# Kernel tuning notes

Hardware: AMD Instinct MI355X
Metric: run time of the kernel (lower is better)

## Reference

```python
import jax, jax.numpy as jnp
import numpy as np

B, S, D = 1, 2048, 2048
H = 16            # num query heads
QL = 1536         # q_lora_rank
KVL = 512         # kv_lora_rank
DN = 128          # qk_nope_head_dim
DR = 64           # qk_rope_head_dim
DV = 128          # v_head_dim
F = 8192          # ffn intermediate
EPS = 1e-6
WAVE = 10000.0


def _rms(x, scale, eps=EPS):
    # fp32 norm then cast back, matching DeepSeekV3_1RMSNorm
    x32 = x.astype(jnp.float32)
    ms = jnp.mean(x32 * x32, axis=-1, keepdims=True)
    return (x32 * jax.lax.rsqrt(ms + eps)).astype(x.dtype) * scale


def _rope_tables(seq_len, dim):
    inv_freq = 1.0 / (WAVE ** (jnp.arange(0, dim, 2, dtype=jnp.float32) / dim))
    t = jnp.arange(seq_len, dtype=jnp.float32)[:, None] * inv_freq[None, :]  # [S, dim/2]
    emb = jnp.concatenate([t, t], axis=-1)  # [S, dim]
    return jnp.cos(emb), jnp.sin(emb)


def _apply_rope(x, cos, sin):
    # x: [B, S, H, dr]; rotate-half convention
    half = x.shape[-1] // 2
    x1, x2 = x[..., :half], x[..., half:]
    rot = jnp.concatenate([-x2, x1], axis=-1)
    return x * cos[None, :, None, :] + rot * sin[None, :, None, :]


def setup_inputs() -> dict:
    key = jax.random.key(0)
    ks = jax.random.split(key, 12)
    w = lambda k, shp: (jax.random.normal(k, shp, dtype=jnp.float32) * 0.02)
    inp = {
        "hidden_states": jax.random.normal(ks[0], (B, S, D), dtype=jnp.float32),
        "attention_mask": jnp.broadcast_to(jnp.tril(jnp.ones((S, S), dtype=bool)), (B, S, S)),
        "pre_attn_scale": jnp.ones((D,), jnp.float32),
        "wqa": w(ks[1], (D, QL)),
        "q_norm_scale": jnp.ones((QL,), jnp.float32),
        "wqb": w(ks[2], (QL, H * (DN + DR))),
        "wkva": w(ks[3], (D, KVL + DR)),
        "kv_norm_scale": jnp.ones((KVL,), jnp.float32),
        "wkvb": w(ks[4], (KVL, H * (DN + DV))),
        "wo": w(ks[5], (H * DV, D)),
        "pre_ffn_scale": jnp.ones((D,), jnp.float32),
        "wg": w(ks[6], (D, F)),
        "bg": jnp.zeros((F,), jnp.float32),
        "wu": w(ks[7], (D, F)),
        "bu": jnp.zeros((F,), jnp.float32),
        "wd": w(ks[8], (F, D)),
        "bd": jnp.zeros((D,), jnp.float32),
    }
    return inp


def reference(hidden_states, attention_mask, pre_attn_scale, wqa, q_norm_scale, wqb,
              wkva, kv_norm_scale, wkvb, wo, pre_ffn_scale, wg, bg, wu, bu, wd, bd):
    x = hidden_states
    # --- pre-attention RMSNorm ---
    n = _rms(x, pre_attn_scale)
    # --- MLA attention ---
    q = (_rms(n @ wqa, q_norm_scale) @ wqb).reshape(B, S, H, DN + DR)
    q_nope, q_rope = q[..., :DN], q[..., DN:]
    kva = n @ wkva                              # [B,S,KVL+DR]
    c_kv, k_rope = kva[..., :KVL], kva[..., KVL:]
    kv = (_rms(c_kv, kv_norm_scale) @ wkvb).reshape(B, S, H, DN + DV)
    k_nope, v = kv[..., :DN], kv[..., DN:]
    cos, sin = _rope_tables(S, DR)
    q_rope = _apply_rope(q_rope, cos, sin)
    k_rope = _apply_rope(k_rope[:, :, None, :], cos, sin)  # [B,S,1,DR] shared across heads
    qf = jnp.concatenate([q_nope, q_rope], axis=-1)
    kf = jnp.concatenate([k_nope, jnp.broadcast_to(k_rope, (B, S, H, DR))], axis=-1)
    scale = 1.0 / float(np.sqrt(DN + DR))
    scores = jnp.einsum('bqhd,bkhd->bhqk', qf, kf) * scale
    scores = jnp.where(attention_mask[:, None, :, :], scores, jnp.float32(-1e9))
    probs = jax.nn.softmax(scores, axis=-1)
    attn = jnp.einsum('bhqk,bkhd->bqhd', probs, v).reshape(B, S, H * DV)
    x = x + attn @ wo                            # residual 1 (dropout=0)
    # --- pre-FFN RMSNorm + dense SwiGLU FFN ---
    n = _rms(x, pre_ffn_scale)
    ff = (jax.nn.silu(n @ wg + bg) * (n @ wu + bu)) @ wd + bd
    return x + ff                                # residual 2
```

## Files before the change

### kernel.cpp

```cpp
#include <hip/hip_runtime.h>
#include <hip/hip_bf16.h>
#include <stdint.h>

typedef unsigned short u16;
using f32x4  = __attribute__((ext_vector_type(4))) float;
using bf16x8 = __attribute__((ext_vector_type(8))) __bf16;
using u32x4  = __attribute__((ext_vector_type(4))) uint32_t;
using u16x4  = __attribute__((ext_vector_type(4))) unsigned short;
using u16x8  = __attribute__((ext_vector_type(8))) unsigned short;

#define S_LEN 2048
#define DM    2048
#define NH    16
#define QLR   1536
#define KVLR  512
#define DNOPE 128
#define DROPE 64
#define DVAL  128
#define FFD   8192

static __device__ __forceinline__ float bf2f(u16 u) {
    union { uint32_t i; float f; } v; v.i = ((uint32_t)u) << 16; return v.f;
}
static __device__ __forceinline__ u16 f2bf(float f) {
    union { float f; uint32_t i; } v; v.f = f;
    uint32_t x = v.i;
    return (u16)((x + 0x7FFF + ((x >> 16) & 1)) >> 16);
}
static __device__ __forceinline__ void gload16(const u16* g, const u16* l) {
    __builtin_amdgcn_global_load_lds(
        (const __attribute__((address_space(1))) void*)g,
        (__attribute__((address_space(3))) void*)l, 16, 0, 0);
}

struct TWJob { const float* src; u16* dst; int R, C, xt, start; };
struct TWJobs { TWJob j[8]; };

__global__ __launch_bounds__(256)
void transpose_all(TWJobs jobs)
{
    __shared__ __align__(16) u16 tile[64][68];
    const int bid = blockIdx.x;
    int e = 0;
#pragma unroll
    for (int i = 1; i < 8; ++i) e = (bid >= jobs.j[i].start) ? i : e;
    const float* src = jobs.j[e].src;
    u16* dst = jobs.j[e].dst;
    const int R = jobs.j[e].R, C = jobs.j[e].C;
    const int local = bid - jobs.j[e].start;
    const int c0 = (local % jobs.j[e].xt) * 64;
    const int r0 = (local / jobs.j[e].xt) * 64;
    const int t = threadIdx.x;
#pragma unroll
    for (int i = 0; i < 4; ++i) {
        int idx = i * 256 + t;
        int r = idx >> 4, c4 = idx & 15;
        float4 v = *reinterpret_cast<const float4*>(&src[(size_t)(r0 + r) * C + c0 + c4 * 4]);
        u16x4 b; b[0] = f2bf(v.x); b[1] = f2bf(v.y); b[2] = f2bf(v.z); b[3] = f2bf(v.w);
        *reinterpret_cast<u16x4*>(&tile[r][c4 * 4]) = b;
    }
    __syncthreads();
#pragma unroll
    for (int i = 0; i < 4; ++i) {
        int idx = i * 256 + t;
        int rr = idx >> 4, k4 = idx & 15;
        u16x4 o;
#pragma unroll
        for (int j = 0; j < 4; ++j) o[j] = tile[k4 * 4 + j][rr];
        *reinterpret_cast<u16x4*>(&dst[(size_t)(c0 + rr) * R + r0 + k4 * 4]) = o;
    }
}

__global__ __launch_bounds__(256)
void transpose_v(const u16* __restrict__ kv, u16* __restrict__ vt)
{
    __shared__ __align__(16) u16 tile[64][76];
    const int t = threadIdx.x;
    const int s0 = blockIdx.x * 64;
    const int d0 = blockIdx.y * 64;
    const int h  = blockIdx.z;
#pragma unroll
    for (int i = 0; i < 2; ++i) {
        int idx = i * 256 + t;
        int s = idx >> 3, c8 = idx & 7;
        u16x8 v = *reinterpret_cast<const u16x8*>(kv + (size_t)(s0 + s) * (NH * 256) + h * 256 + 128 + d0 + c8 * 8);
        u16x4 lo, hi;
#pragma unroll
        for (int j = 0; j < 4; ++j) { lo[j] = v[j]; hi[j] = v[4 + j]; }
        *reinterpret_cast<u16x4*>(&tile[s][c8 * 8])     = lo;
        *reinterpret_cast<u16x4*>(&tile[s][c8 * 8 + 4]) = hi;
    }
    __syncthreads();
#pragma unroll
    for (int i = 0; i < 4; ++i) {
        int idx = i * 256 + t;
        int d = idx >> 4, s4 = idx & 15;
        u16x4 o;
#pragma unroll
        for (int j = 0; j < 4; ++j) o[j] = tile[s4 * 4 + j][d];
        *reinterpret_cast<u16x4*>(&vt[(size_t)(h * 128 + d0 + d) * S_LEN + s0 + s4 * 4]) = o;
    }
}

template<bool IN_F32>
__global__ __launch_bounds__(256)
void rms_norm(const void* __restrict__ in, int in_stride, int width,
              const float* __restrict__ scale, u16* __restrict__ out, int out_stride)
{
    const int row = blockIdx.x;
    const int t = threadIdx.x;
    const float* inf = (const float*)in;
    const u16*   inb = (const u16*)in;
    float ss = 0.f;
    for (int c = t; c < width; c += 256) {
        float v = IN_F32 ? inf[(size_t)row * in_stride + c] : bf2f(inb[(size_t)row * in_stride + c]);
        ss += v * v;
    }
#pragma unroll
    for (int o = 32; o > 0; o >>= 1) ss += __shfl_xor(ss, o);
    __shared__ float red[4];
    if ((t & 63) == 0) red[t >> 6] = ss;
    __syncthreads();
    float inv = rsqrtf((red[0] + red[1] + red[2] + red[3]) / (float)width + 1e-6f);
    for (int c = t; c < width; c += 256) {
        float v = IN_F32 ? inf[(size_t)row * in_stride + c] : bf2f(inb[(size_t)row * in_stride + c]);
        out[(size_t)row * out_stride + c] = f2bf(v * inv * scale[c]);
    }
}

__global__ __launch_bounds__(256)
void rope_qk(u16* __restrict__ q, const float* __restrict__ kva, u16* __restrict__ kr)
{
    const int s = blockIdx.x;
    const int t = threadIdx.x;
    for (int idx = t; idx < 544; idx += 256) {
        int d = idx & 31;
        float invf = powf(10000.f, -(float)(2 * d) / 64.f);
        float ang = (float)s * invf;
        float cs = cosf(ang), sn = sinf(ang);
        if (idx < 512) {
            int hh = idx >> 5;
            u16* base = q + ((size_t)s * NH + hh) * 192 + 128;
            float x1 = bf2f(base[d]), x2 = bf2f(base[d + 32]);
            base[d]      = f2bf(x1 * cs - x2 * sn);
            base[d + 32] = f2bf(x2 * cs + x1 * sn);
        } else {
            const float* kb = kva + (size_t)s * 576 + 512;
            float x1 = kb[d], x2 = kb[d + 32];
            kr[(size_t)s * 64 + d]      = f2bf(x1 * cs - x2 * sn);
            kr[(size_t)s * 64 + d + 32] = f2bf(x2 * cs + x1 * sn);
        }
    }
}

__global__ __launch_bounds__(256)
void init_out(const float* __restrict__ x2, const float* __restrict__ bd,
              float* __restrict__ out, int total4, int N)
{
    int i = blockIdx.x * 256 + threadIdx.x;
    const int stride = gridDim.x * 256;
    for (; i < total4; i += stride) {
        float4 r = ((const float4*)x2)[i];
        int col = (i * 4) & (N - 1);
        float4 b = *reinterpret_cast<const float4*>(&bd[col]);
        float4 o; o.x = r.x + b.x; o.y = r.y + b.y; o.z = r.z + b.z; o.w = r.w + b.w;
        ((float4*)out)[i] = o;
    }
}

__global__ __launch_bounds__(256)
void mul_gu(const u16* __restrict__ g, const u16* __restrict__ u,
            u16* __restrict__ h, int total8)
{
    int i = blockIdx.x * 256 + threadIdx.x;
    const int stride = gridDim.x * 256;
    for (; i < total8; i += stride) {
        u16x8 gv = ((const u16x8*)g)[i];
        u16x8 uv = ((const u16x8*)u)[i];
        u16x8 hv;
#pragma unroll
        for (int j = 0; j < 8; ++j) hv[j] = f2bf(bf2f(gv[j]) * bf2f(uv[j]));
        ((u16x8*)h)[i] = hv;
    }
}

struct GJob { const u16* A; const u16* BT; void* out; int N, K, yCount, zCount; };

template<int EPI>
__global__ __launch_bounds__(256)
void gemm_bt2(GJob j0, GJob j1)
{
    __shared__ __align__(16) u16 As[128 * 64];
    __shared__ __align__(16) u16 Bs[128 * 64];
    const int t = threadIdx.x;
    const int lane = t & 63;
    const int w = t >> 6;
    const int wr = w >> 1, wc = w & 1;
    const int li = lane & 15;
    const int lg = lane >> 4;

    const int gx = gridDim.x;
    int nwg = gx * gridDim.y;
    int bid = blockIdx.y * gx + blockIdx.x;
    bid = (bid & 7) * (nwg >> 3) + (bid >> 3);
    const int m0 = (bid % gx) * 128;
    int yy = bid / gx;

    const int j0span = j0.yCount * j0.zCount;
    const GJob& J = (yy < j0span) ? j0 : j1;
    if (yy >= j0span) yy -= j0span;
    const int ntile = yy % J.yCount;
    const int z = yy / J.yCount;
    const int n0 = ntile * 128;
    const int N = J.N, K = J.K;

    const int nktt = K >> 6;
    const int nz = J.zCount;
    const int qq = nktt / nz, rr = nktt % nz;
    const int kt0 = z * qq + (z < rr ? z : rr);
    const int ktEnd = kt0 + qq + (z < rr ? 1 : 0);

    const int srow = w * 32 + (lane >> 3);
    const int scol = (((lane & 7) ^ (lane >> 3)) << 3);
    const u16* ag = J.A  + (size_t)(m0 + srow) * K + scol;
    const u16* bg = J.BT + (size_t)(n0 + srow) * K + scol;

    f32x4 acc[4][4];
#pragma unroll
    for (int m = 0; m < 4; ++m)
#pragma unroll
        for (int n = 0; n < 4; ++n)
            acc[m][n] = f32x4{0.f, 0.f, 0.f, 0.f};

    for (int kt = kt0; kt < ktEnd; ++kt) {
        const int k0 = kt << 6;
        __syncthreads();
#pragma unroll
        for (int i = 0; i < 4; ++i) {
            gload16(ag + (size_t)i * 8 * K + k0, As + (w * 32 + i * 8) * 64);
            gload16(bg + (size_t)i * 8 * K + k0, Bs + (w * 32 + i * 8) * 64);
        }
        __syncthreads();
#pragma unroll
        for (int kk = 0; kk < 2; ++kk) {
            const int csw = (kk * 32 + lg * 8) ^ ((li & 7) << 3);
            bf16x8 af[4], bfr[4];
#pragma unroll
            for (int m = 0; m < 4; ++m)
                af[m] = *reinterpret_cast<const bf16x8*>(As + (wr * 64 + m * 16 + li) * 64 + csw);
#pragma unroll
            for (int n = 0; n < 4; ++n)
                bfr[n] = *reinterpret_cast<const bf16x8*>(Bs + (wc * 64 + n * 16 + li) * 64 + csw);
#pragma unroll
            for (int m = 0; m < 4; ++m)
#pragma unroll
                for (int n = 0; n < 4; ++n)
                    acc[m][n] = __builtin_amdgcn_mfma_f32_16x16x32_bf16(af[m], bfr[n], acc[m][n], 0, 0, 0);
        }
    }

#pragma unroll
    for (int m = 0; m < 4; ++m) {
        const int row = m0 + wr * 64 + m * 16 + lg * 4;
#pragma unroll
        for (int n = 0; n < 4; ++n) {
            const int col = n0 + wc * 64 + n * 16 + li;
            if (col < N) {
#pragma unroll
                for (int r2 = 0; r2 < 4; ++r2) {
                    float v = acc[m][n][r2];
                    size_t idx = (size_t)(row + r2) * N + col;
                    if (EPI == 0) ((u16*)J.out)[idx] = f2bf(v);
                    else          unsafeAtomicAdd((float*)J.out + idx, v);
                }
            }
        }
    }
}

template<int EPI>
__global__ __launch_bounds__(512, 4)
void gemm_big(const u16* __restrict__ A, const u16* __restrict__ BT,
              void* __restrict__ out, int M, int N, int K,
              const float* __restrict__ bias, const u16* __restrict__ gmul)
{
    __shared__ __align__(16) u16 As[256 * 64];
    __shared__ __align__(16) u16 Bs[128 * 64];
    const int t = threadIdx.x;
    const int lane = t & 63;
    const int w = t >> 6;
    const int wr = w >> 1, wc = w & 1;
    const int li = lane & 15;
    const int lg = lane >> 4;

    const int gx = gridDim.x;
    int nwg = gx * gridDim.y;
    int bid = blockIdx.y * gx + blockIdx.x;
    bid = (bid & 7) * (nwg >> 3) + (bid >> 3);
    const int m0 = (bid % gx) * 256;
    const int n0 = (bid / gx) * 128;

    const int nz = gridDim.z, z = blockIdx.z;
    const int nktt = K >> 6;
    const int qq = nktt / nz, rr = nktt % nz;
    const int kt0 = z * qq + (z < rr ? z : rr);
    const int ktEnd = kt0 + qq + (z < rr ? 1 : 0);

    const int sr = lane >> 3;
    const int scol = (((lane & 7) ^ sr) << 3);
    const u16* ag = A  + (size_t)(m0 + w * 8 + sr) * K + scol;
    const u16* bg = BT + (size_t)(n0 + w * 8 + sr) * K + scol;
    const u16* lA = As + (w * 8) * 64;
    const u16* lB = Bs + (w * 8) * 64;

    f32x4 acc[4][4];
#pragma unroll
    for (int m = 0; m < 4; ++m)
#pragma unroll
        for (int n = 0; n < 4; ++n)
            acc[m][n] = f32x4{0.f, 0.f, 0.f, 0.f};

    for (int kt = kt0; kt < ktEnd; ++kt) {
        const int k0 = kt << 6;
        __syncthreads();
#pragma unroll
        for (int i = 0; i < 4; ++i)
            gload16(ag + (size_t)i * 64 * K + k0, lA + i * 64 * 64);
#pragma unroll
        for (int i = 0; i < 2; ++i)
            gload16(bg + (size_t)i * 64 * K + k0, lB + i * 64 * 64);
        __syncthreads();
        __builtin_amdgcn_s_setprio(1);
#pragma unroll
        for (int kk = 0; kk < 2; ++kk) {
            const int csw = (kk * 32 + lg * 8) ^ ((li & 7) << 3);
            bf16x8 af[4], bfr[4];
#pragma unroll
            for (int m = 0; m < 4; ++m)
                af[m] = *reinterpret_cast<const bf16x8*>(As + (wr * 64 + m * 16 + li) * 64 + csw);
#pragma unroll
            for (int n = 0; n < 4; ++n)
                bfr[n] = *reinterpret_cast<const bf16x8*>(Bs + (wc * 64 + n * 16 + li) * 64 + csw);
#pragma unroll
            for (int m = 0; m < 4; ++m)
#pragma unroll
                for (int n = 0; n < 4; ++n)
                    acc[m][n] = __builtin_amdgcn_mfma_f32_16x16x32_bf16(af[m], bfr[n], acc[m][n], 0, 0, 0);
        }
        __builtin_amdgcn_s_setprio(0);
    }

#pragma unroll
    for (int m = 0; m < 4; ++m) {
        const int row = m0 + wr * 64 + m * 16 + lg * 4;
#pragma unroll
        for (int n = 0; n < 4; ++n) {
            const int col = n0 + wc * 64 + n * 16 + li;
#pragma unroll
            for (int r2 = 0; r2 < 4; ++r2) {
                float v = acc[m][n][r2];
                size_t idx = (size_t)(row + r2) * N + col;
                if (EPI == 0) {
                    ((u16*)out)[idx] = f2bf(v);
                } else if (EPI == 1) {
                    v += bias[col];
                    v = v / (1.f + __expf(-v));
                    ((u16*)out)[idx] = f2bf(v);
                } else {
                    unsafeAtomicAdd((float*)out + idx, v);
                }
            }
        }
    }
}

__global__ __launch_bounds__(512, 4)
void gemm_gu(const u16* __restrict__ A, const u16* __restrict__ BgT, const u16* __restrict__ BuT,
             u16* __restrict__ gout, u16* __restrict__ uout, int M, int N, int K,
             const float* __restrict__ bg, const float* __restrict__ bu)
{
    __shared__ __align__(16) u16 As[256 * 64];
    __shared__ __align__(16) u16 Bs[128 * 64];
    const int t = threadIdx.x;
    const int lane = t & 63;
    const int w = t >> 6;
    const int wr = w >> 1, wc = w & 1;
    const int li = lane & 15;
    const int lg = lane >> 4;
    const int isUp = blockIdx.z;

    const u16* BT = isUp ? BuT : BgT;
    const float* bias = isUp ? bu : bg;
    u16* out = isUp ? uout : gout;

    const int gx = gridDim.x;
    int nwg = gx * gridDim.y;
    int bid = blockIdx.y * gx + blockIdx.x;
    bid = (bid & 7) * (nwg >> 3) + (bid >> 3);
    const int m0 = (bid % gx) * 256;
    const int n0 = (bid / gx) * 128;

    const int sr = lane >> 3;
    const int scol = (((lane & 7) ^ sr) << 3);
    const u16* ag = A  + (size_t)(m0 + w * 8 + sr) * K + scol;
    const u16* bgp = BT + (size_t)(n0 + w * 8 + sr) * K + scol;
    const u16* lA = As + (w * 8) * 64;
    const u16* lB = Bs + (w * 8) * 64;

    f32x4 acc[4][4];
#pragma unroll
    for (int m = 0; m < 4; ++m)
#pragma unroll
        for (int n = 0; n < 4; ++n)
            acc[m][n] = f32x4{0.f, 0.f, 0.f, 0.f};

    const int nkt = K >> 6;
    for (int kt = 0; kt < nkt; ++kt) {
        const int k0 = kt << 6;
        __syncthreads();
#pragma unroll
        for (int i = 0; i < 4; ++i)
            gload16(ag + (size_t)i * 64 * K + k0, lA + i * 64 * 64);
#pragma unroll
        for (int i = 0; i < 2; ++i)
            gload16(bgp + (size_t)i * 64 * K + k0, lB + i * 64 * 64);
        __syncthreads();
        __builtin_amdgcn_s_setprio(1);
#pragma unroll
        for (int kk = 0; kk < 2; ++kk) {
            const int csw = (kk * 32 + lg * 8) ^ ((li & 7) << 3);
            bf16x8 af[4], bfr[4];
#pragma unroll
            for (int m = 0; m < 4; ++m)
                af[m] = *reinterpret_cast<const bf16x8*>(As + (wr * 64 + m * 16 + li) * 64 + csw);
#pragma unroll
            for (int n = 0; n < 4; ++n)
                bfr[n] = *reinterpret_cast<const bf16x8*>(Bs + (wc * 64 + n * 16 + li) * 64 + csw);
#pragma unroll
            for (int m = 0; m < 4; ++m)
#pragma unroll
                for (int n = 0; n < 4; ++n)
                    acc[m][n] = __builtin_amdgcn_mfma_f32_16x16x32_bf16(af[m], bfr[n], acc[m][n], 0, 0, 0);
        }
        __builtin_amdgcn_s_setprio(0);
    }

#pragma unroll
    for (int m = 0; m < 4; ++m) {
        const int row = m0 + wr * 64 + m * 16 + lg * 4;
#pragma unroll
        for (int n = 0; n < 4; ++n) {
            const int col = n0 + wc * 64 + n * 16 + li;
            float bv = bias[col];
#pragma unroll
            for (int r2 = 0; r2 < 4; ++r2) {
                float v = acc[m][n][r2] + bv;
                if (!isUp) v = v / (1.f + __expf(-v));
                ((u16*)out)[(size_t)(row + r2) * N + col] = f2bf(v);
            }
        }
    }
}

__global__ __launch_bounds__(512)
void flash_attn(const u16* __restrict__ q, const u16* __restrict__ kv,
                const u16* __restrict__ kr, const u16* __restrict__ vt,
                u16* __restrict__ attn)
{
    __shared__ __align__(16) u16 KVs[2][20480];
    __shared__ __align__(16) u16 Ps[8][16][72];

    const int t = threadIdx.x;
    const int lane = t & 63;
    const int w = t >> 6;
    const int li = lane & 15;
    const int lg = lane >> 4;
    const int h = blockIdx.x;
    const int b = 15 - blockIdx.y;

    const int qt = (w < 4) ? (2 * b + 1) : (2 * b);
    const int my_nkt = qt + 1;
    const int block_nkt = 2 * b + 2;
    const int wl = w & 3;
    const int qr = qt * 64 + wl * 16;
    const int qpos = qr + li;

    auto stage = [&](int buf, int k0) {
        u16* base = &KVs[buf][0];
#pragma unroll
        for (int i = 0; i < 3; ++i) {
            int g = w * 3 + i;
            int P = g * 64 + lane;
            int j = P / 24, s = P % 24;
            int c = (s & 24) | ((s ^ (j & 7)) & 7);
            const u16* src = (c < 16)
                ? kv + (size_t)(k0 + j) * (NH * 256) + h * 256 + c * 8
                : kr + (size_t)(k0 + j) * 64 + (c - 16) * 8;
            gload16(src, base + g * 512);
        }
#pragma unroll
        for (int i = 0; i < 2; ++i) {
            int g = w * 2 + i;
            int P = g * 64 + lane;
            int d = P >> 3, s8 = P & 7;
            int c = s8 ^ (d & 7);
            const u16* src = vt + (size_t)(h * 128 + d) * S_LEN + k0 + c * 8;
            gload16(src, base + 12288 + g * 512);
        }
    };

    bf16x8 qf[6];
#pragma unroll
    for (int kb = 0; kb < 6; ++kb)
        qf[kb] = *reinterpret_cast<const bf16x8*>(q + ((size_t)(qr + li) * NH + h) * 192 + kb * 32 + lg * 8);

    f32x4 oacc[8];
#pragma unroll
    for (int i = 0; i < 8; ++i) oacc[i] = f32x4{0.f, 0.f, 0.f, 0.f};
    float m_run = -INFINITY, l_run = 0.f;

    stage(0, 0);
    int buf = 0;
    const float scale = 0.07216878364870322f;

    for (int kt = 0; kt < block_nkt; ++kt) {
        const int k0 = kt << 6;
        __syncthreads();
        if (kt + 1 < block_nkt) stage(buf ^ 1, (kt + 1) << 6);

        if (kt < my_nkt) {
            const u16* bb = &KVs[buf][0];

            f32x4 sacc[4];
#pragma unroll
            for (int jt = 0; jt < 4; ++jt) sacc[jt] = f32x4{0.f, 0.f, 0.f, 0.f};
            __builtin_amdgcn_s_setprio(1);
#pragma unroll
            for (int kb = 0; kb < 6; ++kb) {
                const int c = kb * 4 + lg;
                const int s = (c & 24) | ((c ^ (li & 7)) & 7);
#pragma unroll
                for (int jt = 0; jt < 4; ++jt) {
                    bf16x8 kf = *reinterpret_cast<const bf16x8*>(bb + ((jt * 16 + li) * 24 + s) * 8);
                    sacc[jt] = __builtin_amdgcn_mfma_f32_16x16x32_bf16(kf, qf[kb], sacc[jt], 0, 0, 0);
                }
            }
            __builtin_amdgcn_s_setprio(0);

            float p[16];
            float mt = -INFINITY;
            if (k0 + 63 <= qr) {
#pragma unroll
                for (int jt = 0; jt < 4; ++jt)
#pragma unroll
                    for (int r = 0; r < 4; ++r) {
                        float sv = sacc[jt][r] * scale;
                        p[jt * 4 + r] = sv;
                        mt = fmaxf(mt, sv);
                    }
            } else {
#pragma unroll
                for (int jt = 0; jt < 4; ++jt)
#pragma unroll
                    for (int r = 0; r < 4; ++r) {
                        int jpos = k0 + jt * 16 + lg * 4 + r;
                        float sv = (jpos <= qpos) ? sacc[jt][r] * scale : -INFINITY;
                        p[jt * 4 + r] = sv;
                        mt = fmaxf(mt, sv);
                    }
            }
            mt = fmaxf(mt, __shfl_xor(mt, 16));
            mt = fmaxf(mt, __shfl_xor(mt, 32));
            if (!__all(mt <= m_run + 8.f)) {
                float mn = fmaxf(m_run, mt);
                float sf = __expf(m_run - mn);
                float sfr[4];
#pragma unroll
                for (int r = 0; r < 4; ++r)
                    sfr[r] = __shfl(sf, (lane & 48) + lg * 4 + r);
#pragma unroll
                for (int d2 = 0; d2 < 8; ++d2)
#pragma unroll
                    for (int r = 0; r < 4; ++r)
                        oacc[d2][r] *= sfr[r];
                l_run *= sf;
                m_run = mn;
            }
            float rsum = 0.f;
#pragma unroll
            for (int i2 = 0; i2 < 16; ++i2) { p[i2] = __expf(p[i2] - m_run); rsum += p[i2]; }
            rsum += __shfl_xor(rsum, 16);
            rsum += __shfl_xor(rsum, 32);
            l_run += rsum;

#pragma unroll
            for (int jt = 0; jt < 4; ++jt) {
                u16x4 pk;
                pk[0] = f2bf(p[jt * 4 + 0]); pk[1] = f2bf(p[jt * 4 + 1]);
                pk[2] = f2bf(p[jt * 4 + 2]); pk[3] = f2bf(p[jt * 4 + 3]);
                *reinterpret_cast<u16x4*>(&Ps[w][li][jt * 16 + lg * 4]) = pk;
            }

            __builtin_amdgcn_s_setprio(1);
#pragma unroll
            for (int ks = 0; ks < 2; ++ks) {
                bf16x8 pf = *reinterpret_cast<const bf16x8*>(&Ps[w][li][ks * 32 + lg * 8]);
                const int vs = (ks * 4 + lg) ^ (li & 7);
#pragma unroll
                for (int d2 = 0; d2 < 8; ++d2) {
                    bf16x8 vf = *reinterpret_cast<const bf16x8*>(bb + 12288 + ((d2 * 16 + li) * 8 + vs) * 8);
                    oacc[d2] = __builtin_amdgcn_mfma_f32_16x16x32_bf16(pf, vf, oacc[d2], 0, 0, 0);
                }
            }
            __builtin_amdgcn_s_setprio(0);
        }
        buf ^= 1;
    }

    float rl = 1.f / l_run;
    float rlr[4];
#pragma unroll
    for (int r = 0; r < 4; ++r)
        rlr[r] = __shfl(rl, (lane & 48) + lg * 4 + r);
#pragma unroll
    for (int d2 = 0; d2 < 8; ++d2)
#pragma unroll
        for (int r = 0; r < 4; ++r) {
            int srow = qr + lg * 4 + r;
            int dcol = d2 * 16 + li;
            attn[(size_t)srow * (NH * DVAL) + h * DVAL + dcol] = f2bf(oacc[d2][r] * rlr[r]);
        }
}

extern "C" void kernel_launch(void* const* d_in, const int* in_sizes, int n_in,
                              void* d_out, int out_size, void* d_ws, size_t ws_size,
                              hipStream_t stream)
{
    const float* hidden   = (const float*)d_in[0];
    const float* pa_scale = (const float*)d_in[2];
    const float* wqa      = (const float*)d_in[3];
    const float* qn_scale = (const float*)d_in[4];
    const float* wqb      = (const float*)d_in[5];
    const float* wkva     = (const float*)d_in[6];
    const float* kv_scale = (const float*)d_in[7];
    const float* wkvb     = (const float*)d_in[8];
    const float* wo       = (const float*)d_in[9];
    const float* pf_scale = (const float*)d_in[10];
    const float* wg       = (const float*)d_in[11];
    const float* bg       = (const float*)d_in[12];
    const float* wu       = (const float*)d_in[13];
    const float* bu       = (const float*)d_in[14];
    const float* wd       = (const float*)d_in[15];
    const float* bd       = (const float*)d_in[16];
    float* out = (float*)d_out;

    size_t off = 0;
    auto alloc = [&](size_t bytes) {
        off = (off + 255) & ~(size_t)255;
        void* p = (char*)d_ws + off;
        off += bytes;
        return p;
    };
    u16* wqaT  = (u16*)alloc((size_t)QLR * DM * 2);
    u16* wqbT  = (u16*)alloc((size_t)3072 * QLR * 2);
    u16* wkvaT = (u16*)alloc((size_t)640 * DM * 2);
    u16* wkvbT = (u16*)alloc((size_t)4096 * KVLR * 2);
    u16* woT   = (u16*)alloc((size_t)DM * DM * 2);
    u16* wgT   = (u16*)alloc((size_t)FFD * DM * 2);
    u16* wuT   = (u16*)alloc((size_t)FFD * DM * 2);
    u16* wdT   = (u16*)alloc((size_t)DM * FFD * 2);
    u16* n1    = (u16*)alloc((size_t)S_LEN * DM * 2);
    float* qlora32 = (float*)alloc((size_t)S_LEN * QLR * 4);
    float* kva32   = (float*)alloc((size_t)S_LEN * 576 * 4);
    u16* qn    = (u16*)alloc((size_t)S_LEN * QLR * 2);
    u16* qbuf  = (u16*)alloc((size_t)S_LEN * 3072 * 2);
    u16* ckvn  = (u16*)alloc((size_t)S_LEN * KVLR * 2);
    u16* kvbuf = (u16*)alloc((size_t)S_LEN * 4096 * 2);
    u16* krbuf = (u16*)alloc((size_t)S_LEN * 64 * 2);
    u16* attnb = (u16*)alloc((size_t)S_LEN * DM * 2);
    float* x2  = (float*)alloc((size_t)S_LEN * DM * 4);
    u16* n2    = (u16*)alloc((size_t)S_LEN * DM * 2);
    u16* gbuf  = (u16*)alloc((size_t)S_LEN * FFD * 2);
    u16* hbuf  = (u16*)alloc((size_t)S_LEN * FFD * 2);
    u16* vtb  = (u16*)qlora32;
    u16* ubuf = (u16*)qlora32;
    (void)ws_size; (void)in_sizes; (void)n_in; (void)out_size;

    TWJobs jobs;
    int startAcc = 0;
    auto setJob = [&](int i, const float* s, u16* d, int R, int C) {
        jobs.j[i] = TWJob{s, d, R, C, C / 64, startAcc};
        startAcc += (C / 64) * (R / 64);
    };
    setJob(0, wqa,  wqaT,  2048, 1536);
    setJob(1, wqb,  wqbT,  1536, 3072);
    setJob(2, wkva, wkvaT, 2048,  576);
    setJob(3, wkvb, wkvbT,  512, 4096);
    setJob(4, wo,   woT,   2048, 2048);
    setJob(5, wg,   wgT,   2048, 8192);
    setJob(6, wu,   wuT,   2048, 8192);
    setJob(7, wd,   wdT,   8192, 2048);
    hipLaunchKernelGGL(transpose_all, dim3(startAcc), 256, 0, stream, jobs);

    hipMemsetAsync(qlora32, 0, (size_t)S_LEN * QLR * 4, stream);
    hipMemsetAsync(kva32,   0, (size_t)S_LEN * 576 * 4, stream);

    hipLaunchKernelGGL((rms_norm<true>),  dim3(S_LEN), 256, 0, stream, hidden, DM, DM, pa_scale, n1, DM);

    {
        GJob jqa  {n1, wqaT,  qlora32, QLR, DM, 12, 2};
        GJob jkva {n1, wkvaT, kva32,   576, DM,  5, 4};
        hipLaunchKernelGGL((gemm_bt2<5>), dim3(16, 44), 256, 0, stream, jqa, jkva);
    }
    hipLaunchKernelGGL((rms_norm<true>), dim3(S_LEN), 256, 0, stream, qlora32, QLR, QLR, qn_scale, qn, QLR);
    hipLaunchKernelGGL((rms_norm<true>), dim3(S_LEN), 256, 0, stream, kva32, 576, KVLR, kv_scale, ckvn, KVLR);
    {
        GJob jqb  {qn,   wqbT,  qbuf,  3072, QLR,  24, 1};
        GJob jkvb {ckvn, wkvbT, kvbuf, 4096, KVLR, 32, 1};
        hipLaunchKernelGGL((gemm_bt2<0>), dim3(16, 56), 256, 0, stream, jqb, jkvb);
    }
    hipLaunchKernelGGL(rope_qk, dim3(S_LEN), 256, 0, stream, qbuf, kva32, krbuf);

    hipLaunchKernelGGL(transpose_v, dim3(S_LEN/64, 2, NH), 256, 0, stream, kvbuf, vtb);
    hipLaunchKernelGGL(flash_attn, dim3(NH, 16), 512, 0, stream, qbuf, kvbuf, krbuf, vtb, attnb);

    hipMemcpyAsync(x2, hidden, (size_t)S_LEN * DM * 4, hipMemcpyDeviceToDevice, stream);
    hipLaunchKernelGGL((gemm_big<5>), dim3(8, 16, 4), 512, 0, stream, attnb, woT, x2, S_LEN, DM, DM, nullptr, nullptr);

    hipLaunchKernelGGL((rms_norm<true>), dim3(S_LEN), 256, 0, stream, x2, DM, DM, pf_scale, n2, DM);

    hipLaunchKernelGGL(init_out, dim3(2048), 256, 0, stream, x2, bd, out, S_LEN * DM / 4, DM);
    hipLaunchKernelGGL(gemm_gu, dim3(8, 64, 2), 512, 0, stream, n2, wgT, wuT, gbuf, ubuf, S_LEN, FFD, DM, bg, bu);
    hipLaunchKernelGGL(mul_gu, dim3(2048), 256, 0, stream, gbuf, ubuf, hbuf, S_LEN * FFD / 8);
    hipLaunchKernelGGL((gemm_big<5>), dim3(8, 16, 4), 512, 0, stream, hbuf, wdT, out, S_LEN, DM, FFD, nullptr, nullptr);
}
```

Baseline: 660.6 us.

## Overlap late-use weight transposes with flash attention in one fused launch

Moves the transpose and bf16 conversion of wo, wg, wu and wd out of the upfront transpose kernel into extra blocks of the attention kernel. Each extra block transposes eight 64x64 tiles using the attention kernel's shared memory. The attention grid of 256 blocks leaves much of the GPU idle, so the memory-bound transposes can fill those idle CUs instead of running serially. In exchange, attention and transpose blocks compete for bandwidth, and the kernel's LDS footprint may limit co-residency.

```diff
diff --git a/kernel.cpp b/kernel.cpp
--- a/kernel.cpp
+++ b/kernel.cpp
@@ -34,7 +34,7 @@
 }
 
 struct TWJob { const float* src; u16* dst; int R, C, xt, start; };
-struct TWJobs { TWJob j[8]; };
+struct TWJobs { TWJob j[4]; };
 
 __global__ __launch_bounds__(256)
 void transpose_all(TWJobs jobs)
@@ -43,7 +43,7 @@
     const int bid = blockIdx.x;
     int e = 0;
 #pragma unroll
-    for (int i = 1; i < 8; ++i) e = (bid >= jobs.j[i].start) ? i : e;
+    for (int i = 1; i < 4; ++i) e = (bid >= jobs.j[i].start) ? i : e;
     const float* src = jobs.j[e].src;
     u16* dst = jobs.j[e].dst;
     const int R = jobs.j[e].R, C = jobs.j[e].C;
@@ -462,13 +462,56 @@
     }
 }
 
+struct TW4 { const float* src; u16* dst; int R, C, xt, gstart; };
+struct TW4s { TW4 j[4]; };
+
 __global__ __launch_bounds__(512)
-void flash_attn(const u16* __restrict__ q, const u16* __restrict__ kv,
-                const u16* __restrict__ kr, const u16* __restrict__ vt,
-                u16* __restrict__ attn)
-{
-    __shared__ __align__(16) u16 KVs[2][20480];
-    __shared__ __align__(16) u16 Ps[8][16][72];
+void attn_tw(const u16* __restrict__ q, const u16* __restrict__ kv,
+             const u16* __restrict__ kr, const u16* __restrict__ vt,
+             u16* __restrict__ attn, TW4s tj)
+{
+    __shared__ __align__(16) u16 SMEM[2 * 20480 + 8 * 16 * 72];
+
+    if (blockIdx.y >= 16) {
+        u16 (*tile)[68] = reinterpret_cast<u16(*)[68]>(SMEM);
+        const int g = (blockIdx.y - 16) * 16 + blockIdx.x;
+        int e = 0;
+#pragma unroll
+        for (int i = 1; i < 4; ++i) e = (g >= tj.j[i].gstart) ? i : e;
+        const float* src = tj.j[e].src;
+        u16* dst = tj.j[e].dst;
+        const int R = tj.j[e].R, C = tj.j[e].C, xt = tj.j[e].xt;
+        const int base = (g - tj.j[e].gstart) * 8;
+        const int t = threadIdx.x;
+        for (int ti = 0; ti < 8; ++ti) {
+            const int local = base + ti;
+            const int c0 = (local % xt) * 64;
+            const int r0 = (local / xt) * 64;
+            __syncthreads();
+#pragma unroll
+            for (int i = 0; i < 2; ++i) {
+                int idx = i * 512 + t;
+                int r = idx >> 4, c4 = idx & 15;
+                float4 v = *reinterpret_cast<const float4*>(&src[(size_t)(r0 + r) * C + c0 + c4 * 4]);
+                u16x4 b; b[0] = f2bf(v.x); b[1] = f2bf(v.y); b[2] = f2bf(v.z); b[3] = f2bf(v.w);
+                *reinterpret_cast<u16x4*>(&tile[r][c4 * 4]) = b;
+            }
+            __syncthreads();
+#pragma unroll
+            for (int i = 0; i < 2; ++i) {
+                int idx = i * 512 + t;
+                int rr = idx >> 4, k4 = idx & 15;
+                u16x4 o;
+#pragma unroll
+                for (int j = 0; j < 4; ++j) o[j] = tile[k4 * 4 + j][rr];
+                *reinterpret_cast<u16x4*>(&dst[(size_t)(c0 + rr) * R + r0 + k4 * 4]) = o;
+            }
+        }
+        return;
+    }
+
+    u16 (*KVs)[20480] = reinterpret_cast<u16(*)[20480]>(SMEM);
+    u16 (*Ps)[16][72] = reinterpret_cast<u16(*)[16][72]>(SMEM + 2 * 20480);
 
     const int t = threadIdx.x;
     const int lane = t & 63;
@@ -686,21 +729,17 @@
     u16* ubuf = (u16*)qlora32;
     (void)ws_size; (void)in_sizes; (void)n_in; (void)out_size;
 
-    TWJobs jobs;
+    TWJobs ejobs;
     int startAcc = 0;
-    auto setJob = [&](int i, const float* s, u16* d, int R, int C) {
-        jobs.j[i] = TWJob{s, d, R, C, C / 64, startAcc};
+    auto setE = [&](int i, const float* s, u16* d, int R, int C) {
+        ejobs.j[i] = TWJob{s, d, R, C, C / 64, startAcc};
         startAcc += (C / 64) * (R / 64);
     };
-    setJob(0, wqa,  wqaT,  2048, 1536);
-    setJob(1, wqb,  wqbT,  1536, 3072);
-    setJob(2, wkva, wkvaT, 2048,  576);
-    setJob(3, wkvb, wkvbT,  512, 4096);
-    setJob(4, wo,   woT,   2048, 2048);
-    setJob(5, wg,   wgT,   2048, 8192);
-    setJob(6, wu,   wuT,   2048, 8192);
-    setJob(7, wd,   wdT,   8192, 2048);
-    hipLaunchKernelGGL(transpose_all, dim3(startAcc), 256, 0, stream, jobs);
+    setE(0, wqa,  wqaT,  2048, 1536);
+    setE(1, wqb,  wqbT,  1536, 3072);
+    setE(2, wkva, wkvaT, 2048,  576);
+    setE(3, wkvb, wkvbT,  512, 4096);
+    hipLaunchKernelGGL(transpose_all, dim3(startAcc), 256, 0, stream, ejobs);
 
     hipMemsetAsync(qlora32, 0, (size_t)S_LEN * QLR * 4, stream);
     hipMemsetAsync(kva32,   0, (size_t)S_LEN * 576 * 4, stream);
@@ -722,7 +761,18 @@
     hipLaunchKernelGGL(rope_qk, dim3(S_LEN), 256, 0, stream, qbuf, kva32, krbuf);
 
     hipLaunchKernelGGL(transpose_v, dim3(S_LEN/64, 2, NH), 256, 0, stream, kvbuf, vtb);
-    hipLaunchKernelGGL(flash_attn, dim3(NH, 16), 512, 0, stream, qbuf, kvbuf, krbuf, vtb, attnb);
+
+    TW4s tj;
+    int gAcc = 0;
+    auto setL = [&](int i, const float* s, u16* d, int R, int C) {
+        tj.j[i] = TW4{s, d, R, C, C / 64, gAcc};
+        gAcc += (C / 64) * (R / 64) / 8;
+    };
+    setL(0, wo, woT, 2048, 2048);
+    setL(1, wg, wgT, 2048, 8192);
+    setL(2, wu, wuT, 2048, 8192);
+    setL(3, wd, wdT, 8192, 2048);
+    hipLaunchKernelGGL(attn_tw, dim3(16, 16 + 104), 512, 0, stream, qbuf, kvbuf, krbuf, vtb, attnb, tj);
 
     hipMemcpyAsync(x2, hidden, (size_t)S_LEN * DM * 4, hipMemcpyDeviceToDevice, stream);
     hipLaunchKernelGGL((gemm_big<5>), dim3(8, 16, 4), 512, 0, stream, attnb, woT, x2, S_LEN, DM, DM, nullptr, nullptr);
```

New measurement: 625.8 us. -5.3%, faster.
